# Optimization experiments

Hardware: AMD Instinct MI355X
Metric: run time of the kernel (lower is better)

## Reference

```python
import jax, jax.numpy as jnp
import numpy as np

MUL0, MUL1, MUL2, NMOD = 128, 64, 32, 2  # multiplicities of 0e,1e,2e and modalities
D0, D1, D2 = MUL0, MUL1 * 3, MUL2 * 5     # 128, 192, 160 -> total 480


def setup_inputs() -> dict:
    key = jax.random.key(0)
    ks = jax.random.split(key, 7)
    N, G = 200000, 512
    x = jax.random.normal(ks[0], (N, D0 + D1 + D2), dtype=jnp.float32)
    modal_attr = jax.random.uniform(ks[1], (G, NMOD), dtype=jnp.float32)
    W0 = jax.random.normal(ks[2], (MUL0, MUL0), dtype=jnp.float32)
    W0m = jax.random.normal(ks[3], (NMOD, MUL0), dtype=jnp.float32)
    W1 = jax.random.normal(ks[4], (MUL1, MUL1), dtype=jnp.float32)
    W2 = jax.random.normal(ks[5], (MUL2, MUL2), dtype=jnp.float32)
    batch = jnp.sort(jax.random.randint(ks[6], (N,), 0, G, dtype=jnp.int64))
    return {"x": x, "modal_attr": modal_attr, "W0": W0, "W0m": W0m,
            "W1": W1, "W2": W2, "batch": batch}


def reference(x, modal_attr, W0, W0m, W1, W2, batch):
    N = x.shape[0]
    # modality one-hot gathered per node and concatenated (appended 2x0e irrep)
    modal = modal_attr[batch]  # [N, NMOD]
    x0 = x[:, :D0]                                   # [N, 128]  0e
    x1 = x[:, D0:D0 + D1].reshape(N, MUL1, 3)        # [N, 64, 3] 1e
    x2 = x[:, D0 + D1:].reshape(N, MUL2, 5)          # [N, 32, 5] 2e
    # e3nn Linear: per-(l,p) block linear, paths summed, /sqrt(total fan-in mul)
    inv0 = 1.0 / np.sqrt(MUL0 + NMOD).astype(np.float32)
    out0 = (x0 @ W0 + modal @ W0m) * inv0            # [N, 128]
    out1 = jnp.einsum('nim,io->nom', x1, W1) * (1.0 / np.sqrt(MUL1).astype(np.float32))
    out2 = jnp.einsum('nim,io->nom', x2, W2) * (1.0 / np.sqrt(MUL2).astype(np.float32))
    return jnp.concatenate([out0, out1.reshape(N, D1), out2.reshape(N, D2)], axis=1)
```

## Files before the change

### kernel.cpp

```cpp
#include <hip/hip_runtime.h>


typedef __attribute__((ext_vector_type(8))) short  short8;
typedef __attribute__((ext_vector_type(4))) float  f32x4;

#define NTH 256
#define BR  32

#define W0H 0
#define W0L 16384
#define W1H 32768
#define W1L 36864
#define W2H 40960
#define W2L 41984

__device__ __forceinline__ void split_bf16(float v, unsigned short& h, unsigned short& l) {
    unsigned u  = __float_as_uint(v);
    unsigned uh = u & 0xFFFF0000u;
    h = (unsigned short)(uh >> 16);
    float r = v - __uint_as_float(uh);
    unsigned ur = __float_as_uint(r);
    ur += 0x7FFFu + ((ur >> 16) & 1u);
    l = (unsigned short)(ur >> 16);
}

__global__ void prep_weights(const float* __restrict__ W0,
                             const float* __restrict__ W1,
                             const float* __restrict__ W2,
                             unsigned short* __restrict__ ws) {
    const int s0     = blockIdx.x * blockDim.x + threadIdx.x;
    const int STRIDE = gridDim.x * blockDim.x;
    for (int s = s0; s < 16384; s += STRIDE) {
        int j = s & 7, l = (s >> 3) & 63, kt = (s >> 9) & 3, ct = s >> 11;
        int col = ct * 16 + (l & 15);
        int k   = kt * 32 + (l >> 4) * 8 + j;
        unsigned short h, lo;
        split_bf16(W0[k * 128 + col], h, lo);
        ws[W0H + s] = h; ws[W0L + s] = lo;
    }
    for (int s = s0; s < 4096; s += STRIDE) {
        int j = s & 7, l = (s >> 3) & 63, kt = (s >> 9) & 1, ct = s >> 10;
        int col = ct * 16 + (l & 15);
        int k   = kt * 32 + (l >> 4) * 8 + j;
        unsigned short h, lo;
        split_bf16(W1[k * 64 + col], h, lo);
        ws[W1H + s] = h; ws[W1L + s] = lo;
    }
    for (int s = s0; s < 1024; s += STRIDE) {
        int j = s & 7, l = (s >> 3) & 63, ct = s >> 9;
        int col = ct * 16 + (l & 15);
        int k   = (l >> 4) * 8 + j;
        unsigned short h, lo;
        split_bf16(W2[k * 32 + col], h, lo);
        ws[W2H + s] = h; ws[W2L + s] = lo;
    }
}

__device__ __forceinline__ void frag_from_f32(const float* __restrict__ p,
                                              short8& hi, short8& lo) {
    f32x4 a = *reinterpret_cast<const f32x4*>(p);
    f32x4 b = *reinterpret_cast<const f32x4*>(p + 4);
    #pragma unroll
    for (int j = 0; j < 4; ++j) {
        unsigned short h, s;
        split_bf16(a[j], h, s); hi[j]     = (short)h; lo[j]     = (short)s;
        split_bf16(b[j], h, s); hi[4 + j] = (short)h; lo[4 + j] = (short)s;
    }
}

#define MFMA(a, b, c) __builtin_amdgcn_mfma_f32_16x16x32_bf16((a), (b), (c), 0, 0, 0)

__global__ __launch_bounds__(NTH, 4) void irreps_mfma_kernel(
    const float* __restrict__ x,
    const float* __restrict__ modal_attr,
    const float* __restrict__ W0m,
    const unsigned short* __restrict__ wsf,
    const int*   __restrict__ batch,
    float*       __restrict__ out,
    int N)
{
    __shared__ float lds[3 * BR * 68];

    const int tid  = threadIdx.x;
    const int w    = tid >> 6;
    const int l    = tid & 63;
    const int r    = l & 15;
    const int kg   = l >> 4;
    const int rb0  = (w >> 1) * 16;
    const int ch   = w & 1;
    const int row0 = blockIdx.x * BR;
    const int arow = rb0 + r;

    int nr[4]; float am0[4], am1[4];
    #pragma unroll
    for (int reg = 0; reg < 4; ++reg) {
        int n  = row0 + rb0 + kg * 4 + reg;
        nr[reg] = n;
        int nc = n < N ? n : N - 1;
        int g  = batch[nc];
        am0[reg] = modal_attr[2 * g];
        am1[reg] = modal_attr[2 * g + 1];
    }

    const float4* __restrict__ x4 = reinterpret_cast<const float4*>(x);

    #pragma unroll
    for (int k = 0; k < 4; ++k) {
        int idx = tid + k * NTH;
        int rr = idx >> 5, cc = idx & 31;
        int n  = row0 + rr;
        float4 v = x4[(size_t)(n < N ? n : N - 1) * 120 + cc];
        *reinterpret_cast<float4*>(&lds[rr * 132 + cc * 4]) = v;
    }
    __syncthreads();

    {
        short8 ah[4], al[4];
        #pragma unroll
        for (int kt = 0; kt < 4; ++kt)
            frag_from_f32(&lds[arow * 132 + kt * 32 + kg * 8], ah[kt], al[kt]);

        #pragma unroll
        for (int ci = 0; ci < 4; ++ci) {
            int ct = ch * 4 + ci;
            short8 bh[4], bl[4];
            #pragma unroll
            for (int kt = 0; kt < 4; ++kt) {
                int b = ct * 4 + kt;
                bh[kt] = *reinterpret_cast<const short8*>(wsf + W0H + (size_t)(b * 64 + l) * 8);
                bl[kt] = *reinterpret_cast<const short8*>(wsf + W0L + (size_t)(b * 64 + l) * 8);
            }
            f32x4 acc = {0.f, 0.f, 0.f, 0.f};
            #pragma unroll
            for (int kt = 0; kt < 4; ++kt) {
                acc = MFMA(ah[kt], bh[kt], acc);
                acc = MFMA(al[kt], bh[kt], acc);
                acc = MFMA(ah[kt], bl[kt], acc);
            }
            int col = ct * 16 + r;
            float wm0 = W0m[col], wm1 = W0m[128 + col];
            #pragma unroll
            for (int reg = 0; reg < 4; ++reg) {
                if (nr[reg] < N)
                    out[(size_t)nr[reg] * 480 + col] =
                        (acc[reg] + am0[reg] * wm0 + am1[reg] * wm1) * 0.08770580193070293f;
            }
        }
    }
    __syncthreads();

    #pragma unroll
    for (int k = 0; k < 2; ++k) {
        int idx = tid + k * NTH;
        int rr = idx >> 4, ig = idx & 15;
        int n  = row0 + rr;
        const float4* src = &x4[(size_t)(n < N ? n : N - 1) * 120 + 32 + ig * 3];
        float4 f0 = src[0], f1 = src[1], f2 = src[2];
        *reinterpret_cast<float4*>(&lds[(0 * BR + rr) * 68 + ig * 4]) = make_float4(f0.x, f0.w, f1.z, f2.y);
        *reinterpret_cast<float4*>(&lds[(1 * BR + rr) * 68 + ig * 4]) = make_float4(f0.y, f1.x, f1.w, f2.z);
        *reinterpret_cast<float4*>(&lds[(2 * BR + rr) * 68 + ig * 4]) = make_float4(f0.z, f1.y, f2.x, f2.w);
    }
    __syncthreads();

    {
        short8 ah1[3][2], al1[3][2];
        #pragma unroll
        for (int m = 0; m < 3; ++m)
            #pragma unroll
            for (int kt = 0; kt < 2; ++kt)
                frag_from_f32(&lds[(m * BR + arow) * 68 + kt * 32 + kg * 8],
                              ah1[m][kt], al1[m][kt]);

        #pragma unroll
        for (int ci = 0; ci < 2; ++ci) {
            int ct = ch * 2 + ci;
            short8 bh[2], bl[2];
            #pragma unroll
            for (int kt = 0; kt < 2; ++kt) {
                int b = ct * 2 + kt;
                bh[kt] = *reinterpret_cast<const short8*>(wsf + W1H + (size_t)(b * 64 + l) * 8);
                bl[kt] = *reinterpret_cast<const short8*>(wsf + W1L + (size_t)(b * 64 + l) * 8);
            }
            f32x4 accm[3];
            #pragma unroll
            for (int m = 0; m < 3; ++m) {
                f32x4 acc = {0.f, 0.f, 0.f, 0.f};
                #pragma unroll
                for (int kt = 0; kt < 2; ++kt) {
                    acc = MFMA(ah1[m][kt], bh[kt], acc);
                    acc = MFMA(al1[m][kt], bh[kt], acc);
                    acc = MFMA(ah1[m][kt], bl[kt], acc);
                }
                accm[m] = acc;
            }
            int cb = 128 + 3 * (ct * 16 + r);
            #pragma unroll
            for (int reg = 0; reg < 4; ++reg) {
                if (nr[reg] < N) {
                    size_t base = (size_t)nr[reg] * 480 + cb;
                    out[base]     = accm[0][reg] * 0.125f;
                    out[base + 1] = accm[1][reg] * 0.125f;
                    out[base + 2] = accm[2][reg] * 0.125f;
                }
            }
        }
    }
    __syncthreads();

    {
        int rr = tid >> 3, ig = tid & 7;
        int n  = row0 + rr;
        const float4* src = &x4[(size_t)(n < N ? n : N - 1) * 120 + 80 + ig * 5];
        float f[20];
        #pragma unroll
        for (int q = 0; q < 5; ++q) {
            float4 v = src[q];
            f[q * 4 + 0] = v.x; f[q * 4 + 1] = v.y; f[q * 4 + 2] = v.z; f[q * 4 + 3] = v.w;
        }
        #pragma unroll
        for (int m = 0; m < 5; ++m)
            *reinterpret_cast<float4*>(&lds[(m * BR + rr) * 36 + ig * 4]) =
                make_float4(f[m], f[m + 5], f[m + 10], f[m + 15]);
    }
    __syncthreads();

    {
        short8 ah2[5], al2[5];
        #pragma unroll
        for (int m = 0; m < 5; ++m)
            frag_from_f32(&lds[(m * BR + arow) * 36 + kg * 8], ah2[m], al2[m]);

        int ct = ch;
        short8 bh = *reinterpret_cast<const short8*>(wsf + W2H + (size_t)(ct * 64 + l) * 8);
        short8 bl = *reinterpret_cast<const short8*>(wsf + W2L + (size_t)(ct * 64 + l) * 8);

        f32x4 accm[5];
        #pragma unroll
        for (int m = 0; m < 5; ++m) {
            f32x4 acc = {0.f, 0.f, 0.f, 0.f};
            acc = MFMA(ah2[m], bh, acc);
            acc = MFMA(al2[m], bh, acc);
            acc = MFMA(ah2[m], bl, acc);
            accm[m] = acc;
        }
        int cb = 320 + 5 * (ct * 16 + r);
        #pragma unroll
        for (int reg = 0; reg < 4; ++reg) {
            if (nr[reg] < N) {
                size_t base = (size_t)nr[reg] * 480 + cb;
                #pragma unroll
                for (int m = 0; m < 5; ++m)
                    out[base + m] = accm[m][reg] * 0.17677669529663687f;
            }
        }
    }
}

extern "C" void kernel_launch(void* const* d_in, const int* in_sizes, int n_in,
                              void* d_out, int out_size, void* d_ws, size_t ws_size,
                              hipStream_t stream) {
    const float* x     = (const float*)d_in[0];
    const float* modal = (const float*)d_in[1];
    const float* W0    = (const float*)d_in[2];
    const float* W0m   = (const float*)d_in[3];
    const float* W1    = (const float*)d_in[4];
    const float* W2    = (const float*)d_in[5];
    const int*   batch = (const int*)d_in[6];
    float* out = (float*)d_out;
    unsigned short* ws = (unsigned short*)d_ws;

    const int N = in_sizes[6];

    prep_weights<<<84, NTH, 0, stream>>>(W0, W1, W2, ws);

    const int grid = (N + BR - 1) / BR;
    irreps_mfma_kernel<<<grid, NTH, 0, stream>>>(x, modal, W0m, ws, batch, out, N);
}
```

Before: 183.6 us.

## Split fp32 inputs to bf16 hi/lo once at LDS staging with swizzled layout

```diff
diff --git a/kernel.cpp b/kernel.cpp
--- a/kernel.cpp
+++ b/kernel.cpp
@@ -1,4 +1,5 @@
 #include <hip/hip_runtime.h>
+#include <hip/hip_bf16.h>
 
 
 typedef __attribute__((ext_vector_type(8))) short  short8;
@@ -14,14 +15,31 @@
 #define W2H 40960
 #define W2L 41984
 
-__device__ __forceinline__ void split_bf16(float v, unsigned short& h, unsigned short& l) {
-    unsigned u  = __float_as_uint(v);
-    unsigned uh = u & 0xFFFF0000u;
-    h = (unsigned short)(uh >> 16);
-    float r = v - __uint_as_float(uh);
-    unsigned ur = __float_as_uint(r);
-    ur += 0x7FFFu + ((ur >> 16) & 1u);
-    l = (unsigned short)(ur >> 16);
+__device__ __forceinline__ unsigned bc2(__hip_bfloat162 h) {
+    unsigned u; __builtin_memcpy(&u, &h, 4); return u;
+}
+
+struct HL4 { uint2 h, l; };
+
+__device__ __forceinline__ HL4 split4(float a, float b, float c, float d) {
+    __hip_bfloat162 h01 = __float22bfloat162_rn({a, b});
+    __hip_bfloat162 h23 = __float22bfloat162_rn({c, d});
+    float ra = a - __low2float(h01),  rb = b - __high2float(h01);
+    float rc = c - __low2float(h23),  rd = d - __high2float(h23);
+    __hip_bfloat162 l01 = __float22bfloat162_rn({ra, rb});
+    __hip_bfloat162 l23 = __float22bfloat162_rn({rc, rd});
+    HL4 r;
+    r.h = make_uint2(bc2(h01), bc2(h23));
+    r.l = make_uint2(bc2(l01), bc2(l23));
+    return r;
+}
+
+__device__ __forceinline__ void split_w(float v, unsigned short& h, unsigned short& l) {
+    __hip_bfloat16 hb = __float2bfloat16(v);
+    float r = v - __bfloat162float(hb);
+    __hip_bfloat16 lb = __float2bfloat16(r);
+    __builtin_memcpy(&h, &hb, 2);
+    __builtin_memcpy(&l, &lb, 2);
 }
 
 __global__ void prep_weights(const float* __restrict__ W0,
@@ -35,7 +53,7 @@
         int col = ct * 16 + (l & 15);
         int k   = kt * 32 + (l >> 4) * 8 + j;
         unsigned short h, lo;
-        split_bf16(W0[k * 128 + col], h, lo);
+        split_w(W0[k * 128 + col], h, lo);
         ws[W0H + s] = h; ws[W0L + s] = lo;
     }
     for (int s = s0; s < 4096; s += STRIDE) {
@@ -43,7 +61,7 @@
         int col = ct * 16 + (l & 15);
         int k   = kt * 32 + (l >> 4) * 8 + j;
         unsigned short h, lo;
-        split_bf16(W1[k * 64 + col], h, lo);
+        split_w(W1[k * 64 + col], h, lo);
         ws[W1H + s] = h; ws[W1L + s] = lo;
     }
     for (int s = s0; s < 1024; s += STRIDE) {
@@ -51,26 +69,14 @@
         int col = ct * 16 + (l & 15);
         int k   = (l >> 4) * 8 + j;
         unsigned short h, lo;
-        split_bf16(W2[k * 32 + col], h, lo);
+        split_w(W2[k * 32 + col], h, lo);
         ws[W2H + s] = h; ws[W2L + s] = lo;
     }
 }
 
-__device__ __forceinline__ void frag_from_f32(const float* __restrict__ p,
-                                              short8& hi, short8& lo) {
-    f32x4 a = *reinterpret_cast<const f32x4*>(p);
-    f32x4 b = *reinterpret_cast<const f32x4*>(p + 4);
-    #pragma unroll
-    for (int j = 0; j < 4; ++j) {
-        unsigned short h, s;
-        split_bf16(a[j], h, s); hi[j]     = (short)h; lo[j]     = (short)s;
-        split_bf16(b[j], h, s); hi[4 + j] = (short)h; lo[4 + j] = (short)s;
-    }
-}
-
 #define MFMA(a, b, c) __builtin_amdgcn_mfma_f32_16x16x32_bf16((a), (b), (c), 0, 0, 0)
 
-__global__ __launch_bounds__(NTH, 4) void irreps_mfma_kernel(
+__global__ __launch_bounds__(NTH, 5) void irreps_mfma_kernel(
     const float* __restrict__ x,
     const float* __restrict__ modal_attr,
     const float* __restrict__ W0m,
@@ -79,7 +85,8 @@
     float*       __restrict__ out,
     int N)
 {
-    __shared__ float lds[3 * BR * 68];
+    __shared__ __align__(16) unsigned short lds[12288];
+    char* ldsb = reinterpret_cast<char*>(lds);
 
     const int tid  = threadIdx.x;
     const int w    = tid >> 6;
@@ -104,38 +111,45 @@
 
     const float4* __restrict__ x4 = reinterpret_cast<const float4*>(x);
 
-    #pragma unroll
-    for (int k = 0; k < 4; ++k) {
-        int idx = tid + k * NTH;
-        int rr = idx >> 5, cc = idx & 31;
-        int n  = row0 + rr;
-        float4 v = x4[(size_t)(n < N ? n : N - 1) * 120 + cc];
-        *reinterpret_cast<float4*>(&lds[rr * 132 + cc * 4]) = v;
-    }
-    __syncthreads();
-
-    {
+    {
+        const int seg = tid & 15;
+        const int rr0 = tid >> 4;
+        #pragma unroll
+        for (int t2 = 0; t2 < 2; ++t2) {
+            int rr = rr0 + 16 * t2;
+            int n  = row0 + rr; n = n < N ? n : N - 1;
+            const float4* src = &x4[(size_t)n * 120 + seg * 2];
+            float4 a = src[0], b = src[1];
+            HL4 p = split4(a.x, a.y, a.z, a.w);
+            HL4 q = split4(b.x, b.y, b.z, b.w);
+            int byte = (rr * 256 + seg * 16) ^ ((rr & 7) << 4);
+            *reinterpret_cast<uint4*>(ldsb + byte)        = make_uint4(p.h.x, p.h.y, q.h.x, q.h.y);
+            *reinterpret_cast<uint4*>(ldsb + 8192 + byte) = make_uint4(p.l.x, p.l.y, q.l.x, q.l.y);
+        }
+    }
+    __syncthreads();
+
+    {
+        const int sw = (arow & 7) << 4;
         short8 ah[4], al[4];
         #pragma unroll
-        for (int kt = 0; kt < 4; ++kt)
-            frag_from_f32(&lds[arow * 132 + kt * 32 + kg * 8], ah[kt], al[kt]);
-
+        for (int kt = 0; kt < 4; ++kt) {
+            int byte = (arow * 256 + kt * 64 + kg * 16) ^ sw;
+            ah[kt] = *reinterpret_cast<const short8*>(ldsb + byte);
+            al[kt] = *reinterpret_cast<const short8*>(ldsb + 8192 + byte);
+        }
         #pragma unroll
         for (int ci = 0; ci < 4; ++ci) {
             int ct = ch * 4 + ci;
-            short8 bh[4], bl[4];
+            f32x4 acc = {0.f, 0.f, 0.f, 0.f};
             #pragma unroll
             for (int kt = 0; kt < 4; ++kt) {
                 int b = ct * 4 + kt;
-                bh[kt] = *reinterpret_cast<const short8*>(wsf + W0H + (size_t)(b * 64 + l) * 8);
-                bl[kt] = *reinterpret_cast<const short8*>(wsf + W0L + (size_t)(b * 64 + l) * 8);
-            }
-            f32x4 acc = {0.f, 0.f, 0.f, 0.f};
-            #pragma unroll
-            for (int kt = 0; kt < 4; ++kt) {
-                acc = MFMA(ah[kt], bh[kt], acc);
-                acc = MFMA(al[kt], bh[kt], acc);
-                acc = MFMA(ah[kt], bl[kt], acc);
+                short8 bh = *reinterpret_cast<const short8*>(wsf + W0H + (size_t)(b * 64 + l) * 8);
+                short8 bl = *reinterpret_cast<const short8*>(wsf + W0L + (size_t)(b * 64 + l) * 8);
+                acc = MFMA(ah[kt], bh, acc);
+                acc = MFMA(al[kt], bh, acc);
+                acc = MFMA(ah[kt], bl, acc);
             }
             int col = ct * 16 + r;
             float wm0 = W0m[col], wm1 = W0m[128 + col];
@@ -149,58 +163,58 @@
     }
     __syncthreads();
 
-    #pragma unroll
-    for (int k = 0; k < 2; ++k) {
-        int idx = tid + k * NTH;
-        int rr = idx >> 4, ig = idx & 15;
-        int n  = row0 + rr;
-        const float4* src = &x4[(size_t)(n < N ? n : N - 1) * 120 + 32 + ig * 3];
-        float4 f0 = src[0], f1 = src[1], f2 = src[2];
-        *reinterpret_cast<float4*>(&lds[(0 * BR + rr) * 68 + ig * 4]) = make_float4(f0.x, f0.w, f1.z, f2.y);
-        *reinterpret_cast<float4*>(&lds[(1 * BR + rr) * 68 + ig * 4]) = make_float4(f0.y, f1.x, f1.w, f2.z);
-        *reinterpret_cast<float4*>(&lds[(2 * BR + rr) * 68 + ig * 4]) = make_float4(f0.z, f1.y, f2.x, f2.w);
-    }
-    __syncthreads();
-
-    {
-        short8 ah1[3][2], al1[3][2];
-        #pragma unroll
-        for (int m = 0; m < 3; ++m)
-            #pragma unroll
-            for (int kt = 0; kt < 2; ++kt)
-                frag_from_f32(&lds[(m * BR + arow) * 68 + kt * 32 + kg * 8],
-                              ah1[m][kt], al1[m][kt]);
-
-        #pragma unroll
-        for (int ci = 0; ci < 2; ++ci) {
-            int ct = ch * 2 + ci;
-            short8 bh[2], bl[2];
+    {
+        const int ig  = tid & 15;
+        const int rr0 = tid >> 4;
+        #pragma unroll
+        for (int t2 = 0; t2 < 2; ++t2) {
+            int rr = rr0 + 16 * t2;
+            int n  = row0 + rr; n = n < N ? n : N - 1;
+            const float4* src = &x4[(size_t)n * 120 + 32 + ig * 3];
+            float4 f0 = src[0], f1 = src[1], f2 = src[2];
+            HL4 s0 = split4(f0.x, f0.w, f1.z, f2.y);
+            HL4 s1 = split4(f0.y, f1.x, f1.w, f2.z);
+            HL4 s2 = split4(f0.z, f1.y, f2.x, f2.w);
+            int rbyte = (rr * 128 + ig * 8) ^ ((rr & 7) << 4);
+            *reinterpret_cast<uint2*>(ldsb + 0 * 4096 + rbyte)         = s0.h;
+            *reinterpret_cast<uint2*>(ldsb + 1 * 4096 + rbyte)         = s1.h;
+            *reinterpret_cast<uint2*>(ldsb + 2 * 4096 + rbyte)         = s2.h;
+            *reinterpret_cast<uint2*>(ldsb + 12288 + 0 * 4096 + rbyte) = s0.l;
+            *reinterpret_cast<uint2*>(ldsb + 12288 + 1 * 4096 + rbyte) = s1.l;
+            *reinterpret_cast<uint2*>(ldsb + 12288 + 2 * 4096 + rbyte) = s2.l;
+        }
+    }
+    __syncthreads();
+
+    {
+        const int sw = (arow & 7) << 4;
+        #pragma unroll
+        for (int m = 0; m < 3; ++m) {
+            short8 ah[2], al[2];
             #pragma unroll
             for (int kt = 0; kt < 2; ++kt) {
-                int b = ct * 2 + kt;
-                bh[kt] = *reinterpret_cast<const short8*>(wsf + W1H + (size_t)(b * 64 + l) * 8);
-                bl[kt] = *reinterpret_cast<const short8*>(wsf + W1L + (size_t)(b * 64 + l) * 8);
-            }
-            f32x4 accm[3];
-            #pragma unroll
-            for (int m = 0; m < 3; ++m) {
+                int byte = (arow * 128 + kt * 64 + kg * 16) ^ sw;
+                ah[kt] = *reinterpret_cast<const short8*>(ldsb + m * 4096 + byte);
+                al[kt] = *reinterpret_cast<const short8*>(ldsb + 12288 + m * 4096 + byte);
+            }
+            #pragma unroll
+            for (int ci = 0; ci < 2; ++ci) {
+                int ct = ch * 2 + ci;
                 f32x4 acc = {0.f, 0.f, 0.f, 0.f};
                 #pragma unroll
                 for (int kt = 0; kt < 2; ++kt) {
-                    acc = MFMA(ah1[m][kt], bh[kt], acc);
-                    acc = MFMA(al1[m][kt], bh[kt], acc);
-                    acc = MFMA(ah1[m][kt], bl[kt], acc);
+                    int b = ct * 2 + kt;
+                    short8 bh = *reinterpret_cast<const short8*>(wsf + W1H + (size_t)(b * 64 + l) * 8);
+                    short8 bl = *reinterpret_cast<const short8*>(wsf + W1L + (size_t)(b * 64 + l) * 8);
+                    acc = MFMA(ah[kt], bh, acc);
+                    acc = MFMA(al[kt], bh, acc);
+                    acc = MFMA(ah[kt], bl, acc);
                 }
-                accm[m] = acc;
-            }
-            int cb = 128 + 3 * (ct * 16 + r);
-            #pragma unroll
-            for (int reg = 0; reg < 4; ++reg) {
-                if (nr[reg] < N) {
-                    size_t base = (size_t)nr[reg] * 480 + cb;
-                    out[base]     = accm[0][reg] * 0.125f;
-                    out[base + 1] = accm[1][reg] * 0.125f;
-                    out[base + 2] = accm[2][reg] * 0.125f;
+                int cb = 128 + 3 * (ct * 16 + r) + m;
+                #pragma unroll
+                for (int reg = 0; reg < 4; ++reg) {
+                    if (nr[reg] < N)
+                        out[(size_t)nr[reg] * 480 + cb] = acc[reg] * 0.125f;
                 }
             }
         }
@@ -209,48 +223,43 @@
 
     {
         int rr = tid >> 3, ig = tid & 7;
-        int n  = row0 + rr;
-        const float4* src = &x4[(size_t)(n < N ? n : N - 1) * 120 + 80 + ig * 5];
+        int n  = row0 + rr; n = n < N ? n : N - 1;
+        const float4* src = &x4[(size_t)n * 120 + 80 + ig * 5];
         float f[20];
         #pragma unroll
         for (int q = 0; q < 5; ++q) {
             float4 v = src[q];
             f[q * 4 + 0] = v.x; f[q * 4 + 1] = v.y; f[q * 4 + 2] = v.z; f[q * 4 + 3] = v.w;
         }
-        #pragma unroll
-        for (int m = 0; m < 5; ++m)
-            *reinterpret_cast<float4*>(&lds[(m * BR + rr) * 36 + ig * 4]) =
-                make_float4(f[m], f[m + 5], f[m + 10], f[m + 15]);
-    }
-    __syncthreads();
-
-    {
-        short8 ah2[5], al2[5];
-        #pragma unroll
-        for (int m = 0; m < 5; ++m)
-            frag_from_f32(&lds[(m * BR + arow) * 36 + kg * 8], ah2[m], al2[m]);
-
+        int rbyte = (rr * 64 + ig * 8) ^ ((rr & 3) << 4);
+        #pragma unroll
+        for (int m = 0; m < 5; ++m) {
+            HL4 s = split4(f[m], f[5 + m], f[10 + m], f[15 + m]);
+            *reinterpret_cast<uint2*>(ldsb + m * 2048 + rbyte)         = s.h;
+            *reinterpret_cast<uint2*>(ldsb + 10240 + m * 2048 + rbyte) = s.l;
+        }
+    }
+    __syncthreads();
+
+    {
+        const int sw2 = (arow & 3) << 4;
         int ct = ch;
         short8 bh = *reinterpret_cast<const short8*>(wsf + W2H + (size_t)(ct * 64 + l) * 8);
         short8 bl = *reinterpret_cast<const short8*>(wsf + W2L + (size_t)(ct * 64 + l) * 8);
-
-        f32x4 accm[5];
         #pragma unroll
         for (int m = 0; m < 5; ++m) {
+            int byte = (arow * 64 + kg * 16) ^ sw2;
+            short8 ah = *reinterpret_cast<const short8*>(ldsb + m * 2048 + byte);
+            short8 al = *reinterpret_cast<const short8*>(ldsb + 10240 + m * 2048 + byte);
             f32x4 acc = {0.f, 0.f, 0.f, 0.f};
-            acc = MFMA(ah2[m], bh, acc);
-            acc = MFMA(al2[m], bh, acc);
-            acc = MFMA(ah2[m], bl, acc);
-            accm[m] = acc;
-        }
-        int cb = 320 + 5 * (ct * 16 + r);
-        #pragma unroll
-        for (int reg = 0; reg < 4; ++reg) {
-            if (nr[reg] < N) {
-                size_t base = (size_t)nr[reg] * 480 + cb;
-                #pragma unroll
-                for (int m = 0; m < 5; ++m)
-                    out[base + m] = accm[m][reg] * 0.17677669529663687f;
+            acc = MFMA(ah, bh, acc);
+            acc = MFMA(al, bh, acc);
+            acc = MFMA(ah, bl, acc);
+            int cb = 320 + 5 * (ct * 16 + r) + m;
+            #pragma unroll
+            for (int reg = 0; reg < 4; ++reg) {
+                if (nr[reg] < N)
+                    out[(size_t)nr[reg] * 480 + cb] = acc[reg] * 0.17677669529663687f;
             }
         }
     }
```

Measured after the change: 216.7 us. 1.18x slower.
